# Performance work log

Measured on AMD Instinct MI355X. Metric: run time of the kernel, lower is better.

## Reference

```python
import jax, jax.numpy as jnp
import numpy as np

NUM_NODES = 100000
NUM_EDGES = 1600000
NUM_GRAPHS = 512
IN_F = 128
BN_EPS = 1e-5


def setup_inputs() -> dict:
    key = jax.random.key(0)
    ks = jax.random.split(key, 8)
    x = jax.random.normal(ks[0], (NUM_NODES, IN_F), dtype=jnp.float32)
    edge_index = jax.random.randint(ks[1], (2, NUM_EDGES), 0, NUM_NODES, dtype=jnp.int64)
    batch = jnp.sort(jax.random.randint(ks[2], (NUM_NODES,), 0, NUM_GRAPHS, dtype=jnp.int64))

    def glorot(k, shape):
        lim = np.sqrt(6.0 / (shape[0] + shape[1]))
        return jax.random.uniform(k, shape, jnp.float32, -lim, lim)

    return {
        "x": x,
        "edge_index": edge_index,
        "batch": batch,
        "W1": glorot(ks[3], (IN_F, 128)),
        "b1": jnp.zeros((128,), jnp.float32),
        "W2": glorot(ks[4], (128, 64)),
        "b2": jnp.zeros((64,), jnp.float32),
        "gamma": jnp.ones((64,), jnp.float32),
        "beta": jnp.zeros((64,), jnp.float32),
        "Wo1": glorot(ks[5], (64, 24)),
        "bo1": jnp.zeros((24,), jnp.float32),
        "Wo2": glorot(ks[6], (24, 1)),
        "bo2": jnp.zeros((1,), jnp.float32),
    }


def gcn_conv(x, src, dst, W, b, n):
    # PyG GCNConv: add self-loops, symmetric D^{-1/2} A D^{-1/2} normalization,
    # linear transform, scatter-add aggregation at destination, then bias.
    deg = jax.ops.segment_sum(jnp.ones_like(dst, jnp.float32), dst, num_segments=n)
    dis = jnp.where(deg > 0, jax.lax.rsqrt(deg), 0.0)
    norm = dis[src] * dis[dst]  # [E+N]
    xw = x @ W                  # [N, out]
    msg = xw[src] * norm[:, None]
    return jax.ops.segment_sum(msg, dst, num_segments=n) + b


def reference(x, edge_index, batch, W1, b1, W2, b2, gamma, beta, Wo1, bo1, Wo2, bo2):
    n = NUM_NODES
    loop = jnp.arange(n, dtype=edge_index.dtype)
    src = jnp.concatenate([edge_index[0], loop])  # self-loops appended
    dst = jnp.concatenate([edge_index[1], loop])

    h1 = jax.nn.relu(gcn_conv(x, src, dst, W1, b1, n))
    h2 = jax.nn.relu(gcn_conv(h1, src, dst, W2, b2, n))

    pooled = jax.ops.segment_sum(h2, batch, num_segments=NUM_GRAPHS)  # [G, 64]
    h = jax.lax.stop_gradient(pooled)

    # BatchNorm1d in training mode: batch statistics over the graph dim.
    mean = jnp.mean(pooled, axis=0)
    var = jnp.var(pooled, axis=0)
    xn = (pooled - mean) * jax.lax.rsqrt(var + BN_EPS) * gamma + beta

    out = jax.nn.relu(xn @ Wo1 + bo1) @ Wo2 + bo2  # [G, 1]
    return out, h
```

## Files before the change

### kernel.cpp

```cpp
#include <hip/hip_runtime.h>
#include <math.h>

#define N_NODES 100000
#define N_EDGES 1600000
#define N_GRAPHS 512
#define BN_EPS 1e-5f

#define NBUCKET 1024
#define NBUCKET_USED ((N_NODES + 127) / 128)
#define BCHUNK 8192
#define NCHUNKS ((N_EDGES + BCHUNK - 1) / BCHUNK)

typedef unsigned int uint;
typedef unsigned short ushort;
typedef _Float16 f16;
typedef _Float16 f16x8 __attribute__((ext_vector_type(8)));
typedef float f32x4 __attribute__((ext_vector_type(4)));

constexpr size_t OFF_BCNT  = 0;
constexpr size_t OFF_BCUR  = 4096;
constexpr size_t OFF_BBASE = 8192;
constexpr size_t OFF_DIS   = 12288;
constexpr size_t OFF_ROW   = 412288;
constexpr size_t OFF_SC    = 812416;
constexpr size_t OFF_SH    = 812672;
constexpr size_t OFF_WT    = 812928;
constexpr size_t OFF_CSR   = 862080;
constexpr size_t OFF_P     = 7262080;
constexpr size_t OFF_Q     = 32862080;

__device__ __forceinline__ uint packf16(float a, float b) {
    union { f16 h[2]; uint u; } z;
    z.h[0] = (f16)a; z.h[1] = (f16)b;
    return z.u;
}
__device__ __forceinline__ float2 unpackf16(uint u) {
    union { uint u; f16 h[2]; } z;
    z.u = u;
    return make_float2((float)z.h[0], (float)z.h[1]);
}

__global__ __launch_bounds__(256) void bucket_hist(const int* __restrict__ dst,
                                                   int* __restrict__ bcnt) {
    __shared__ int h[NBUCKET];
    for (int i = threadIdx.x; i < NBUCKET; i += 256) h[i] = 0;
    __syncthreads();
    int stride = gridDim.x * 256;
    for (int e = blockIdx.x * 256 + threadIdx.x; e < N_EDGES; e += stride)
        atomicAdd(&h[dst[e] >> 7], 1);
    __syncthreads();
    for (int i = threadIdx.x; i < NBUCKET; i += 256) {
        int v = h[i];
        if (v) atomicAdd(&bcnt[i], v);
    }
}

__global__ __launch_bounds__(1024) void scan_buckets(const int* __restrict__ bcnt,
                                                     int* __restrict__ bcur,
                                                     int* __restrict__ bbase) {
    __shared__ int tmp[NBUCKET];
    int t = threadIdx.x;
    int c = bcnt[t];
    tmp[t] = c;
    __syncthreads();
    for (int off = 1; off < NBUCKET; off <<= 1) {
        int add = (t >= off) ? tmp[t - off] : 0;
        __syncthreads();
        tmp[t] += add;
        __syncthreads();
    }
    bcur[t] = tmp[t] - c;
    bbase[t] = tmp[t] - c;
}

__global__ __launch_bounds__(1024) void bin_scatter(const int* __restrict__ src,
                                                    const int* __restrict__ dst,
                                                    int* __restrict__ bcur,
                                                    uint* __restrict__ binned) {
    constexpr int REG = BCHUNK / 1024;
    __shared__ int hist[NBUCKET];
    __shared__ int base[NBUCKET];
    int t = threadIdx.x;
    int e0 = blockIdx.x * BCHUNK;
    int lim = N_EDGES - e0;

    hist[t] = 0;
    __syncthreads();

    int ds[REG], ss[REG];
#pragma unroll
    for (int i = 0; i < REG; ++i) {
        int idx = t + i * 1024;
        if (idx < lim) {
            ds[i] = dst[e0 + idx];
            ss[i] = src[e0 + idx];
            atomicAdd(&hist[ds[i] >> 7], 1);
        }
    }
    __syncthreads();

    int h = hist[t];
    base[t] = h ? atomicAdd(&bcur[t], h) : 0;
    hist[t] = 0;
    __syncthreads();

#pragma unroll
    for (int i = 0; i < REG; ++i) {
        int idx = t + i * 1024;
        if (idx < lim) {
            int b = ds[i] >> 7;
            int pos = base[b] + atomicAdd(&hist[b], 1);
            binned[pos] = ((uint)ss[i] << 7) | (uint)(ds[i] & 127);
        }
    }
}

__global__ __launch_bounds__(256) void csr_from_bins(const uint* __restrict__ binned,
                                                     const int* __restrict__ bbase,
                                                     const int* __restrict__ bcnt,
                                                     int* __restrict__ row_start,
                                                     float* __restrict__ dis,
                                                     int* __restrict__ csr_src) {
    __shared__ int cnt[128];
    __shared__ int ex[128];
    int t = threadIdx.x;
    int b = blockIdx.x;
    if (t < 128) cnt[t] = 0;
    __syncthreads();
    int start = bbase[b];
    int end = start + bcnt[b];
    for (int i = start + t; i < end; i += 256)
        atomicAdd(&cnt[binned[i] & 127u], 1);
    __syncthreads();
    if (t < 128) ex[t] = cnt[t];
    __syncthreads();
    for (int off = 1; off < 128; off <<= 1) {
        int v = (t < 128 && t >= off) ? ex[t - off] : 0;
        __syncthreads();
        if (t < 128) ex[t] += v;
        __syncthreads();
    }
    if (t < 128) {
        int c = cnt[t];
        ex[t] -= c;
        int node = b * 128 + t;
        if (node < N_NODES) {
            row_start[node] = start + ex[t];
            dis[node] = rsqrtf((float)(c + 1));
        }
        cnt[t] = 0;
    }
    if (b == 0 && t == 0) row_start[N_NODES] = N_EDGES;
    __syncthreads();
    for (int i = start + t; i < end; i += 256) {
        uint p = binned[i];
        int s = (int)(p >> 7);
        int d = (int)(p & 127u);
        int pos = start + ex[d] + atomicAdd(&cnt[d], 1);
        csr_src[pos] = s;
    }
}

__global__ __launch_bounds__(256) void prep_w(const float* __restrict__ W1,
                                              const float* __restrict__ W2,
                                              f16* __restrict__ wT) {
    int tid = blockIdx.x * 256 + threadIdx.x;
    if (tid < 16384) {
        int n = tid >> 7, k = tid & 127;
        wT[tid] = (f16)W1[k * 128 + n];
    } else if (tid < 24576) {
        int t = tid - 16384;
        int n = t >> 7, k = t & 127;
        wT[tid] = (f16)W2[k * 64 + n];
    }
}

__global__ __launch_bounds__(256) void gemm_mfma1(const float* __restrict__ X,
                                                  const float* __restrict__ dis,
                                                  const f16* __restrict__ Bt,
                                                  ushort* __restrict__ Y) {
    constexpr int NT = 8;
    constexpr int PITCH = 136;
    __shared__ f16 sA[64 * PITCH];
    __shared__ f16 sB[128 * PITCH];
    int tid = threadIdx.x;
    int n0 = blockIdx.x * 64;

    for (int i = tid; i < 64 * 16; i += 256) {
        int r = i >> 4, c = i & 15;
        int n = n0 + r;
        uint4 pk = make_uint4(0, 0, 0, 0);
        if (n < N_NODES) {
            const float4* px = (const float4*)(X + (size_t)n * 128);
            float4 u = px[c * 2], v = px[c * 2 + 1];
            float d = dis[n];
            pk.x = packf16(u.x * d, u.y * d);
            pk.y = packf16(u.z * d, u.w * d);
            pk.z = packf16(v.x * d, v.y * d);
            pk.w = packf16(v.z * d, v.w * d);
        }
        *(uint4*)&sA[r * PITCH + c * 8] = pk;
    }
    for (int i = tid; i < 128 * 16; i += 256) {
        int r = i >> 4, c = i & 15;
        *(uint4*)&sB[r * PITCH + c * 8] = ((const uint4*)(Bt + r * 128))[c];
    }
    __syncthreads();

    int lane = tid & 63, wave = tid >> 6;
    int l15 = lane & 15, q = lane >> 4;
    int m0 = wave * 16;
    f32x4 acc[NT];
#pragma unroll
    for (int nt = 0; nt < NT; ++nt) acc[nt] = (f32x4){0.f, 0.f, 0.f, 0.f};

    const f16* pa = &sA[(m0 + l15) * PITCH + q * 8];
    const f16* pb = &sB[l15 * PITCH + q * 8];
#pragma unroll
    for (int kk = 0; kk < 4; ++kk) {
        f16x8 a = *(const f16x8*)(pa + kk * 32);
#pragma unroll
        for (int nt = 0; nt < NT; ++nt) {
            f16x8 b = *(const f16x8*)(pb + nt * 16 * PITCH + kk * 32);
            acc[nt] = __builtin_amdgcn_mfma_f32_16x16x32_f16(a, b, acc[nt], 0, 0, 0);
        }
    }

    int row_base = n0 + m0 + q * 4;
#pragma unroll
    for (int nt = 0; nt < NT; ++nt) {
#pragma unroll
        for (int r = 0; r < 4; ++r) {
            int row = row_base + r;
            if (row < N_NODES) {
                union { f16 h; ushort u; } z;
                z.h = (f16)acc[nt][r];
                Y[(size_t)row * 128 + nt * 16 + l15] = z.u;
            }
        }
    }
}

template <int OUTF>
__global__ __launch_bounds__(256) void gemm_mfma(const f16* __restrict__ A,
                                                 const f16* __restrict__ Bt,
                                                 ushort* __restrict__ Y) {
    constexpr int NT = OUTF / 16;
    constexpr int PITCH = 136;
    __shared__ f16 sA[64 * PITCH];
    __shared__ f16 sB[OUTF * PITCH];
    int tid = threadIdx.x;
    int n0 = blockIdx.x * 64;

    for (int i = tid; i < 64 * 16; i += 256) {
        int r = i >> 4, c = i & 15;
        int n = n0 + r;
        uint4 v = make_uint4(0, 0, 0, 0);
        if (n < N_NODES) v = ((const uint4*)(A + (size_t)n * 128))[c];
        *(uint4*)&sA[r * PITCH + c * 8] = v;
    }
    for (int i = tid; i < OUTF * 16; i += 256) {
        int r = i >> 4, c = i & 15;
        *(uint4*)&sB[r * PITCH + c * 8] = ((const uint4*)(Bt + r * 128))[c];
    }
    __syncthreads();

    int lane = tid & 63, wave = tid >> 6;
    int l15 = lane & 15, q = lane >> 4;
    int m0 = wave * 16;
    f32x4 acc[NT];
#pragma unroll
    for (int nt = 0; nt < NT; ++nt) acc[nt] = (f32x4){0.f, 0.f, 0.f, 0.f};

    const f16* pa = &sA[(m0 + l15) * PITCH + q * 8];
    const f16* pb = &sB[l15 * PITCH + q * 8];
#pragma unroll
    for (int kk = 0; kk < 4; ++kk) {
        f16x8 a = *(const f16x8*)(pa + kk * 32);
#pragma unroll
        for (int nt = 0; nt < NT; ++nt) {
            f16x8 b = *(const f16x8*)(pb + nt * 16 * PITCH + kk * 32);
            acc[nt] = __builtin_amdgcn_mfma_f32_16x16x32_f16(a, b, acc[nt], 0, 0, 0);
        }
    }

    int row_base = n0 + m0 + q * 4;
#pragma unroll
    for (int nt = 0; nt < NT; ++nt) {
#pragma unroll
        for (int r = 0; r < 4; ++r) {
            int row = row_base + r;
            if (row < N_NODES) {
                union { f16 h; ushort u; } z;
                z.h = (f16)acc[nt][r];
                Y[(size_t)row * OUTF + nt * 16 + l15] = z.u;
            }
        }
    }
}

__global__ __launch_bounds__(256) void aggregate1(const ushort* __restrict__ M,
                                                  const int* __restrict__ row_start,
                                                  const int* __restrict__ csr_src,
                                                  const float* __restrict__ dis,
                                                  const float* __restrict__ bias,
                                                  ushort* __restrict__ H1s) {
    int wv = __builtin_amdgcn_readfirstlane((int)(threadIdx.x >> 6));
    int n = blockIdx.x * 4 + wv;
    if (n >= N_NODES) return;
    int lane = threadIdx.x & 63;
    float dn = dis[n];
    int e0 = row_start[n], e1 = row_start[n + 1];
    const uint* rows = (const uint*)M;
    float2 t0 = unpackf16(rows[(size_t)n * 64 + lane]);
    float a0 = t0.x, a1 = t0.y, b0 = 0.f, b1v = 0.f;
    int e = e0;
    for (; e + 16 <= e1; e += 16) {
        int s[16];
#pragma unroll
        for (int j = 0; j < 16; ++j) s[j] = csr_src[e + j];
        uint v[16];
#pragma unroll
        for (int j = 0; j < 16; ++j) v[j] = rows[(size_t)s[j] * 64 + lane];
#pragma unroll
        for (int j = 0; j < 16; ++j) {
            float2 f = unpackf16(v[j]);
            if (j & 1) { b0 += f.x; b1v += f.y; } else { a0 += f.x; a1 += f.y; }
        }
    }
    for (; e + 8 <= e1; e += 8) {
        int s[8];
#pragma unroll
        for (int j = 0; j < 8; ++j) s[j] = csr_src[e + j];
        uint v[8];
#pragma unroll
        for (int j = 0; j < 8; ++j) v[j] = rows[(size_t)s[j] * 64 + lane];
#pragma unroll
        for (int j = 0; j < 8; ++j) {
            float2 f = unpackf16(v[j]);
            if (j & 1) { b0 += f.x; b1v += f.y; } else { a0 += f.x; a1 += f.y; }
        }
    }
    for (; e + 4 <= e1; e += 4) {
        int s0 = csr_src[e], s1 = csr_src[e + 1], s2 = csr_src[e + 2], s3 = csr_src[e + 3];
        uint v0 = rows[(size_t)s0 * 64 + lane];
        uint v1 = rows[(size_t)s1 * 64 + lane];
        uint v2 = rows[(size_t)s2 * 64 + lane];
        uint v3 = rows[(size_t)s3 * 64 + lane];
        float2 f0 = unpackf16(v0), f1 = unpackf16(v1), f2 = unpackf16(v2), f3 = unpackf16(v3);
        a0 += f0.x + f1.x; a1 += f0.y + f1.y;
        b0 += f2.x + f3.x; b1v += f2.y + f3.y;
    }
    for (; e < e1; ++e) {
        float2 f = unpackf16(rows[(size_t)csr_src[e] * 64 + lane]);
        a0 += f.x; a1 += f.y;
    }
    a0 += b0; a1 += b1v;
    a0 = fmaxf(fmaf(a0, dn, bias[2 * lane]), 0.f) * dn;
    a1 = fmaxf(fmaf(a1, dn, bias[2 * lane + 1]), 0.f) * dn;
    ((uint*)H1s)[(size_t)n * 64 + lane] = packf16(a0, a1);
}

__global__ __launch_bounds__(256) void aggregate2(const ushort* __restrict__ M,
                                                  const int* __restrict__ row_start,
                                                  const int* __restrict__ csr_src,
                                                  const float* __restrict__ dis,
                                                  const float* __restrict__ bias,
                                                  float* __restrict__ out) {
    int wv = __builtin_amdgcn_readfirstlane((int)(threadIdx.x >> 6));
    int n = blockIdx.x * 4 + wv;
    if (n >= N_NODES) return;
    int lane = threadIdx.x & 63;
    float dn = dis[n];
    int e0 = row_start[n], e1 = row_start[n + 1];
    const f16* rows = (const f16*)M;
    float a0 = (float)rows[(size_t)n * 64 + lane];
    float a1 = 0.f;
    int e = e0;
    for (; e + 16 <= e1; e += 16) {
        int s[16];
#pragma unroll
        for (int j = 0; j < 16; ++j) s[j] = csr_src[e + j];
        f16 v[16];
#pragma unroll
        for (int j = 0; j < 16; ++j) v[j] = rows[(size_t)s[j] * 64 + lane];
#pragma unroll
        for (int j = 0; j < 16; ++j) {
            if (j & 1) a1 += (float)v[j]; else a0 += (float)v[j];
        }
    }
    for (; e + 8 <= e1; e += 8) {
        int s[8];
#pragma unroll
        for (int j = 0; j < 8; ++j) s[j] = csr_src[e + j];
        f16 v[8];
#pragma unroll
        for (int j = 0; j < 8; ++j) v[j] = rows[(size_t)s[j] * 64 + lane];
#pragma unroll
        for (int j = 0; j < 8; ++j) {
            if (j & 1) a1 += (float)v[j]; else a0 += (float)v[j];
        }
    }
    for (; e + 4 <= e1; e += 4) {
        int s0 = csr_src[e], s1 = csr_src[e + 1], s2 = csr_src[e + 2], s3 = csr_src[e + 3];
        float v0 = (float)rows[(size_t)s0 * 64 + lane];
        float v1 = (float)rows[(size_t)s1 * 64 + lane];
        float v2 = (float)rows[(size_t)s2 * 64 + lane];
        float v3 = (float)rows[(size_t)s3 * 64 + lane];
        a0 += v0 + v1; a1 += v2 + v3;
    }
    for (; e < e1; ++e) a0 += (float)rows[(size_t)csr_src[e] * 64 + lane];
    a0 += a1;
    a0 = fmaf(a0, dn, bias[lane]);
    out[(size_t)n * 64 + lane] = fmaxf(a0, 0.f);
}

__global__ __launch_bounds__(64) void pool_graphs(const float* __restrict__ H,
                                                  const int* __restrict__ batch,
                                                  float* __restrict__ pooled) {
    int g = blockIdx.x;
    int lane = threadIdx.x;
    int lo = 0, hi = N_NODES;
    while (lo < hi) { int mid = (lo + hi) >> 1; if (batch[mid] < g) lo = mid + 1; else hi = mid; }
    int start = lo;
    hi = N_NODES;
    while (lo < hi) { int mid = (lo + hi) >> 1; if (batch[mid] < g + 1) lo = mid + 1; else hi = mid; }
    int end = lo;
    float a0 = 0.f, a1 = 0.f;
    int i = start;
    for (; i + 4 <= end; i += 4) {
        a0 += H[(size_t)i * 64 + lane] + H[(size_t)(i + 1) * 64 + lane];
        a1 += H[(size_t)(i + 2) * 64 + lane] + H[(size_t)(i + 3) * 64 + lane];
    }
    for (; i < end; ++i) a0 += H[(size_t)i * 64 + lane];
    pooled[g * 64 + lane] = a0 + a1;
}

__global__ __launch_bounds__(64) void bn_stats(const float* __restrict__ pooled,
                                               const float* __restrict__ gamma,
                                               const float* __restrict__ beta,
                                               float* __restrict__ scale,
                                               float* __restrict__ shift) {
    int f = threadIdx.x;
    float s = 0.f, s2 = 0.f;
    for (int g = 0; g < N_GRAPHS; ++g) {
        float v = pooled[g * 64 + f];
        s += v;
        s2 = fmaf(v, v, s2);
    }
    float mean = s * (1.0f / N_GRAPHS);
    float var = s2 * (1.0f / N_GRAPHS) - mean * mean;
    float istd = rsqrtf(var + BN_EPS);
    float sc = gamma[f] * istd;
    scale[f] = sc;
    shift[f] = beta[f] - mean * sc;
}

__global__ __launch_bounds__(256) void head(const float* __restrict__ pooled,
                                            const float* __restrict__ scale,
                                            const float* __restrict__ shift,
                                            const float* __restrict__ Wo1,
                                            const float* __restrict__ bo1,
                                            const float* __restrict__ Wo2,
                                            const float* __restrict__ bo2,
                                            float* __restrict__ out) {
    __shared__ float sW1[64 * 24];
    __shared__ float sW2[24];
    __shared__ float sb1[24];
    __shared__ float ssc[64];
    __shared__ float ssh[64];
    int tid = threadIdx.x;
    for (int i = tid; i < 64 * 24; i += 256) sW1[i] = Wo1[i];
    if (tid < 24) { sW2[tid] = Wo2[tid]; sb1[tid] = bo1[tid]; }
    if (tid < 64) { ssc[tid] = scale[tid]; ssh[tid] = shift[tid]; }
    __syncthreads();
    int g = blockIdx.x * 256 + tid;
    if (g >= N_GRAPHS) return;
    float xn[64];
    const float* pr = pooled + g * 64;
#pragma unroll
    for (int j = 0; j < 64; ++j) xn[j] = fmaf(pr[j], ssc[j], ssh[j]);
    float o = bo2[0];
#pragma unroll 4
    for (int k = 0; k < 24; ++k) {
        float h = sb1[k];
#pragma unroll
        for (int j = 0; j < 64; ++j) h = fmaf(xn[j], sW1[j * 24 + k], h);
        o = fmaf(fmaxf(h, 0.f), sW2[k], o);
    }
    out[g] = o;
}

extern "C" void kernel_launch(void* const* d_in, const int* in_sizes, int n_in,
                              void* d_out, int out_size, void* d_ws, size_t ws_size,
                              hipStream_t stream) {
    const float* x     = (const float*)d_in[0];
    const int*   ei    = (const int*)d_in[1];
    const int*   batch = (const int*)d_in[2];
    const float* W1    = (const float*)d_in[3];
    const float* b1    = (const float*)d_in[4];
    const float* W2    = (const float*)d_in[5];
    const float* b2    = (const float*)d_in[6];
    const float* gamma = (const float*)d_in[7];
    const float* beta  = (const float*)d_in[8];
    const float* Wo1   = (const float*)d_in[9];
    const float* bo1   = (const float*)d_in[10];
    const float* Wo2   = (const float*)d_in[11];
    const float* bo2   = (const float*)d_in[12];
    float* out = (float*)d_out;
    char* ws = (char*)d_ws;

    const int* srcv = ei;
    const int* dstv = ei + N_EDGES;
    int*    bcnt     = (int*)(ws + OFF_BCNT);
    int*    bcur     = (int*)(ws + OFF_BCUR);
    int*    bbase    = (int*)(ws + OFF_BBASE);
    float*  dis      = (float*)(ws + OFF_DIS);
    int*    row_start= (int*)(ws + OFF_ROW);
    float*  scale    = (float*)(ws + OFF_SC);
    float*  shift    = (float*)(ws + OFF_SH);
    f16*    wT       = (f16*)(ws + OFF_WT);
    int*    csr_src  = (int*)(ws + OFF_CSR);
    f16*    bufP     = (f16*)(ws + OFF_P);
    ushort* bufQ     = (ushort*)(ws + OFF_Q);
    uint*   binned   = (uint*)(ws + OFF_Q);
    float*  pooled   = out + N_GRAPHS;

    hipMemsetAsync(ws + OFF_BCNT, 0, 4096, stream);

    bucket_hist<<<256, 256, 0, stream>>>(dstv, bcnt);
    scan_buckets<<<1, NBUCKET, 0, stream>>>(bcnt, bcur, bbase);
    bin_scatter<<<NCHUNKS, 1024, 0, stream>>>(srcv, dstv, bcur, binned);
    csr_from_bins<<<NBUCKET_USED, 256, 0, stream>>>(binned, bbase, bcnt, row_start, dis, csr_src);

    prep_w<<<96, 256, 0, stream>>>(W1, W2, wT);

    int gblocks = (N_NODES + 63) / 64;
    int ablocks = (N_NODES + 3) / 4;
    gemm_mfma1<<<gblocks, 256, 0, stream>>>(x, dis, wT, bufQ);
    aggregate1<<<ablocks, 256, 0, stream>>>(bufQ, row_start, csr_src, dis, b1, (ushort*)bufP);
    gemm_mfma<64><<<gblocks, 256, 0, stream>>>(bufP, wT + 16384, bufQ);
    aggregate2<<<ablocks, 256, 0, stream>>>(bufQ, row_start, csr_src, dis, b2, (float*)bufP);

    pool_graphs<<<N_GRAPHS, 64, 0, stream>>>((float*)bufP, batch, pooled);
    bn_stats<<<1, 64, 0, stream>>>(pooled, gamma, beta, scale, shift);
    head<<<2, 256, 0, stream>>>(pooled, scale, shift, Wo1, bo1, Wo2, bo2, out);
}
```

Baseline: 336.0 us.

## Fuse layer-1 aggregation with layer-2 GEMM and merge BN stats into head

```diff
diff --git a/kernel.cpp b/kernel.cpp
--- a/kernel.cpp
+++ b/kernel.cpp
@@ -22,8 +22,6 @@
 constexpr size_t OFF_BBASE = 8192;
 constexpr size_t OFF_DIS   = 12288;
 constexpr size_t OFF_ROW   = 412288;
-constexpr size_t OFF_SC    = 812416;
-constexpr size_t OFF_SH    = 812672;
 constexpr size_t OFF_WT    = 812928;
 constexpr size_t OFF_CSR   = 862080;
 constexpr size_t OFF_P     = 7262080;
@@ -241,124 +239,99 @@
     }
 }
 
-template <int OUTF>
-__global__ __launch_bounds__(256) void gemm_mfma(const f16* __restrict__ A,
-                                                 const f16* __restrict__ Bt,
-                                                 ushort* __restrict__ Y) {
-    constexpr int NT = OUTF / 16;
+__global__ __launch_bounds__(256) void aggregate1_fused(const ushort* __restrict__ M,
+                                                        const int* __restrict__ row_start,
+                                                        const int* __restrict__ csr_src,
+                                                        const float* __restrict__ dis,
+                                                        const float* __restrict__ bias,
+                                                        const f16* __restrict__ W2t,
+                                                        ushort* __restrict__ M2) {
     constexpr int PITCH = 136;
-    __shared__ f16 sA[64 * PITCH];
-    __shared__ f16 sB[OUTF * PITCH];
+    constexpr int HP = 130;
+    __shared__ f16 sB[64 * PITCH];
+    __shared__ f16 sH[16 * HP];
     int tid = threadIdx.x;
-    int n0 = blockIdx.x * 64;
-
     for (int i = tid; i < 64 * 16; i += 256) {
         int r = i >> 4, c = i & 15;
+        *(uint4*)&sB[r * PITCH + c * 8] = ((const uint4*)(W2t + r * 128))[c];
+    }
+    int wv = __builtin_amdgcn_readfirstlane((int)(tid >> 6));
+    int lane = tid & 63;
+    int n0 = blockIdx.x * 16;
+    const uint* rows = (const uint*)M;
+
+    for (int i = 0; i < 4; ++i) {
+        int r = wv * 4 + i;
         int n = n0 + r;
-        uint4 v = make_uint4(0, 0, 0, 0);
-        if (n < N_NODES) v = ((const uint4*)(A + (size_t)n * 128))[c];
-        *(uint4*)&sA[r * PITCH + c * 8] = v;
-    }
-    for (int i = tid; i < OUTF * 16; i += 256) {
-        int r = i >> 4, c = i & 15;
-        *(uint4*)&sB[r * PITCH + c * 8] = ((const uint4*)(Bt + r * 128))[c];
-    }
-    __syncthreads();
-
-    int lane = tid & 63, wave = tid >> 6;
+        float dn = dis[n];
+        int e0 = row_start[n], e1 = row_start[n + 1];
+        float2 t0 = unpackf16(rows[(size_t)n * 64 + lane]);
+        float a0 = t0.x, a1 = t0.y, b0 = 0.f, b1v = 0.f;
+        int e = e0;
+        for (; e + 16 <= e1; e += 16) {
+            int s[16];
+#pragma unroll
+            for (int j = 0; j < 16; ++j) s[j] = csr_src[e + j];
+            uint v[16];
+#pragma unroll
+            for (int j = 0; j < 16; ++j) v[j] = rows[(size_t)s[j] * 64 + lane];
+#pragma unroll
+            for (int j = 0; j < 16; ++j) {
+                float2 f = unpackf16(v[j]);
+                if (j & 1) { b0 += f.x; b1v += f.y; } else { a0 += f.x; a1 += f.y; }
+            }
+        }
+        for (; e + 8 <= e1; e += 8) {
+            int s[8];
+#pragma unroll
+            for (int j = 0; j < 8; ++j) s[j] = csr_src[e + j];
+            uint v[8];
+#pragma unroll
+            for (int j = 0; j < 8; ++j) v[j] = rows[(size_t)s[j] * 64 + lane];
+#pragma unroll
+            for (int j = 0; j < 8; ++j) {
+                float2 f = unpackf16(v[j]);
+                if (j & 1) { b0 += f.x; b1v += f.y; } else { a0 += f.x; a1 += f.y; }
+            }
+        }
+        for (; e + 4 <= e1; e += 4) {
+            int s0 = csr_src[e], s1 = csr_src[e + 1], s2 = csr_src[e + 2], s3 = csr_src[e + 3];
+            uint v0 = rows[(size_t)s0 * 64 + lane];
+            uint v1 = rows[(size_t)s1 * 64 + lane];
+            uint v2 = rows[(size_t)s2 * 64 + lane];
+            uint v3 = rows[(size_t)s3 * 64 + lane];
+            float2 f0 = unpackf16(v0), f1 = unpackf16(v1), f2 = unpackf16(v2), f3 = unpackf16(v3);
+            a0 += f0.x + f1.x; a1 += f0.y + f1.y;
+            b0 += f2.x + f3.x; b1v += f2.y + f3.y;
+        }
+        for (; e < e1; ++e) {
+            float2 f = unpackf16(rows[(size_t)csr_src[e] * 64 + lane]);
+            a0 += f.x; a1 += f.y;
+        }
+        a0 += b0; a1 += b1v;
+        a0 = fmaxf(fmaf(a0, dn, bias[2 * lane]), 0.f) * dn;
+        a1 = fmaxf(fmaf(a1, dn, bias[2 * lane + 1]), 0.f) * dn;
+        *(uint*)&sH[r * HP + 2 * lane] = packf16(a0, a1);
+    }
+    __syncthreads();
+
     int l15 = lane & 15, q = lane >> 4;
-    int m0 = wave * 16;
-    f32x4 acc[NT];
-#pragma unroll
-    for (int nt = 0; nt < NT; ++nt) acc[nt] = (f32x4){0.f, 0.f, 0.f, 0.f};
-
-    const f16* pa = &sA[(m0 + l15) * PITCH + q * 8];
-    const f16* pb = &sB[l15 * PITCH + q * 8];
+    f32x4 acc = (f32x4){0.f, 0.f, 0.f, 0.f};
+    const f16* pa = &sH[l15 * HP + q * 8];
+    const f16* pb = &sB[(wv * 16 + l15) * PITCH + q * 8];
 #pragma unroll
     for (int kk = 0; kk < 4; ++kk) {
         f16x8 a = *(const f16x8*)(pa + kk * 32);
-#pragma unroll
-        for (int nt = 0; nt < NT; ++nt) {
-            f16x8 b = *(const f16x8*)(pb + nt * 16 * PITCH + kk * 32);
-            acc[nt] = __builtin_amdgcn_mfma_f32_16x16x32_f16(a, b, acc[nt], 0, 0, 0);
-        }
-    }
-
-    int row_base = n0 + m0 + q * 4;
-#pragma unroll
-    for (int nt = 0; nt < NT; ++nt) {
-#pragma unroll
-        for (int r = 0; r < 4; ++r) {
-            int row = row_base + r;
-            if (row < N_NODES) {
-                union { f16 h; ushort u; } z;
-                z.h = (f16)acc[nt][r];
-                Y[(size_t)row * OUTF + nt * 16 + l15] = z.u;
-            }
-        }
-    }
-}
-
-__global__ __launch_bounds__(256) void aggregate1(const ushort* __restrict__ M,
-                                                  const int* __restrict__ row_start,
-                                                  const int* __restrict__ csr_src,
-                                                  const float* __restrict__ dis,
-                                                  const float* __restrict__ bias,
-                                                  ushort* __restrict__ H1s) {
-    int wv = __builtin_amdgcn_readfirstlane((int)(threadIdx.x >> 6));
-    int n = blockIdx.x * 4 + wv;
-    if (n >= N_NODES) return;
-    int lane = threadIdx.x & 63;
-    float dn = dis[n];
-    int e0 = row_start[n], e1 = row_start[n + 1];
-    const uint* rows = (const uint*)M;
-    float2 t0 = unpackf16(rows[(size_t)n * 64 + lane]);
-    float a0 = t0.x, a1 = t0.y, b0 = 0.f, b1v = 0.f;
-    int e = e0;
-    for (; e + 16 <= e1; e += 16) {
-        int s[16];
-#pragma unroll
-        for (int j = 0; j < 16; ++j) s[j] = csr_src[e + j];
-        uint v[16];
-#pragma unroll
-        for (int j = 0; j < 16; ++j) v[j] = rows[(size_t)s[j] * 64 + lane];
-#pragma unroll
-        for (int j = 0; j < 16; ++j) {
-            float2 f = unpackf16(v[j]);
-            if (j & 1) { b0 += f.x; b1v += f.y; } else { a0 += f.x; a1 += f.y; }
-        }
-    }
-    for (; e + 8 <= e1; e += 8) {
-        int s[8];
-#pragma unroll
-        for (int j = 0; j < 8; ++j) s[j] = csr_src[e + j];
-        uint v[8];
-#pragma unroll
-        for (int j = 0; j < 8; ++j) v[j] = rows[(size_t)s[j] * 64 + lane];
-#pragma unroll
-        for (int j = 0; j < 8; ++j) {
-            float2 f = unpackf16(v[j]);
-            if (j & 1) { b0 += f.x; b1v += f.y; } else { a0 += f.x; a1 += f.y; }
-        }
-    }
-    for (; e + 4 <= e1; e += 4) {
-        int s0 = csr_src[e], s1 = csr_src[e + 1], s2 = csr_src[e + 2], s3 = csr_src[e + 3];
-        uint v0 = rows[(size_t)s0 * 64 + lane];
-        uint v1 = rows[(size_t)s1 * 64 + lane];
-        uint v2 = rows[(size_t)s2 * 64 + lane];
-        uint v3 = rows[(size_t)s3 * 64 + lane];
-        float2 f0 = unpackf16(v0), f1 = unpackf16(v1), f2 = unpackf16(v2), f3 = unpackf16(v3);
-        a0 += f0.x + f1.x; a1 += f0.y + f1.y;
-        b0 += f2.x + f3.x; b1v += f2.y + f3.y;
-    }
-    for (; e < e1; ++e) {
-        float2 f = unpackf16(rows[(size_t)csr_src[e] * 64 + lane]);
-        a0 += f.x; a1 += f.y;
-    }
-    a0 += b0; a1 += b1v;
-    a0 = fmaxf(fmaf(a0, dn, bias[2 * lane]), 0.f) * dn;
-    a1 = fmaxf(fmaf(a1, dn, bias[2 * lane + 1]), 0.f) * dn;
-    ((uint*)H1s)[(size_t)n * 64 + lane] = packf16(a0, a1);
+        f16x8 b = *(const f16x8*)(pb + kk * 32);
+        acc = __builtin_amdgcn_mfma_f32_16x16x32_f16(a, b, acc, 0, 0, 0);
+    }
+    int row_base = n0 + q * 4;
+#pragma unroll
+    for (int rr = 0; rr < 4; ++rr) {
+        union { f16 h; ushort u; } z;
+        z.h = (f16)acc[rr];
+        M2[(size_t)(row_base + rr) * 64 + wv * 16 + l15] = z.u;
+    }
 }
 
 __global__ __launch_bounds__(256) void aggregate2(const ushort* __restrict__ M,
@@ -436,46 +409,38 @@
     pooled[g * 64 + lane] = a0 + a1;
 }
 
-__global__ __launch_bounds__(64) void bn_stats(const float* __restrict__ pooled,
+__global__ __launch_bounds__(512) void bn_head(const float* __restrict__ pooled,
                                                const float* __restrict__ gamma,
                                                const float* __restrict__ beta,
-                                               float* __restrict__ scale,
-                                               float* __restrict__ shift) {
-    int f = threadIdx.x;
-    float s = 0.f, s2 = 0.f;
-    for (int g = 0; g < N_GRAPHS; ++g) {
-        float v = pooled[g * 64 + f];
-        s += v;
-        s2 = fmaf(v, v, s2);
-    }
-    float mean = s * (1.0f / N_GRAPHS);
-    float var = s2 * (1.0f / N_GRAPHS) - mean * mean;
-    float istd = rsqrtf(var + BN_EPS);
-    float sc = gamma[f] * istd;
-    scale[f] = sc;
-    shift[f] = beta[f] - mean * sc;
-}
-
-__global__ __launch_bounds__(256) void head(const float* __restrict__ pooled,
-                                            const float* __restrict__ scale,
-                                            const float* __restrict__ shift,
-                                            const float* __restrict__ Wo1,
-                                            const float* __restrict__ bo1,
-                                            const float* __restrict__ Wo2,
-                                            const float* __restrict__ bo2,
-                                            float* __restrict__ out) {
+                                               const float* __restrict__ Wo1,
+                                               const float* __restrict__ bo1,
+                                               const float* __restrict__ Wo2,
+                                               const float* __restrict__ bo2,
+                                               float* __restrict__ out) {
     __shared__ float sW1[64 * 24];
     __shared__ float sW2[24];
     __shared__ float sb1[24];
     __shared__ float ssc[64];
     __shared__ float ssh[64];
     int tid = threadIdx.x;
-    for (int i = tid; i < 64 * 24; i += 256) sW1[i] = Wo1[i];
-    if (tid < 24) { sW2[tid] = Wo2[tid]; sb1[tid] = bo1[tid]; }
-    if (tid < 64) { ssc[tid] = scale[tid]; ssh[tid] = shift[tid]; }
-    __syncthreads();
-    int g = blockIdx.x * 256 + tid;
-    if (g >= N_GRAPHS) return;
+    for (int i = tid; i < 64 * 24; i += 512) sW1[i] = Wo1[i];
+    if (tid >= 64 && tid < 88) { int k = tid - 64; sW2[k] = Wo2[k]; sb1[k] = bo1[k]; }
+    if (tid < 64) {
+        float s = 0.f, s2 = 0.f;
+        for (int g = 0; g < N_GRAPHS; ++g) {
+            float v = pooled[g * 64 + tid];
+            s += v;
+            s2 = fmaf(v, v, s2);
+        }
+        float mean = s * (1.0f / N_GRAPHS);
+        float var = s2 * (1.0f / N_GRAPHS) - mean * mean;
+        float istd = rsqrtf(var + BN_EPS);
+        float sc = gamma[tid] * istd;
+        ssc[tid] = sc;
+        ssh[tid] = beta[tid] - mean * sc;
+    }
+    __syncthreads();
+    int g = tid;
     float xn[64];
     const float* pr = pooled + g * 64;
 #pragma unroll
@@ -517,11 +482,9 @@
     int*    bbase    = (int*)(ws + OFF_BBASE);
     float*  dis      = (float*)(ws + OFF_DIS);
     int*    row_start= (int*)(ws + OFF_ROW);
-    float*  scale    = (float*)(ws + OFF_SC);
-    float*  shift    = (float*)(ws + OFF_SH);
     f16*    wT       = (f16*)(ws + OFF_WT);
     int*    csr_src  = (int*)(ws + OFF_CSR);
-    f16*    bufP     = (f16*)(ws + OFF_P);
+    ushort* bufP     = (ushort*)(ws + OFF_P);
     ushort* bufQ     = (ushort*)(ws + OFF_Q);
     uint*   binned   = (uint*)(ws + OFF_Q);
     float*  pooled   = out + N_GRAPHS;
@@ -536,13 +499,12 @@
     prep_w<<<96, 256, 0, stream>>>(W1, W2, wT);
 
     int gblocks = (N_NODES + 63) / 64;
-    int ablocks = (N_NODES + 3) / 4;
     gemm_mfma1<<<gblocks, 256, 0, stream>>>(x, dis, wT, bufQ);
-    aggregate1<<<ablocks, 256, 0, stream>>>(bufQ, row_start, csr_src, dis, b1, (ushort*)bufP);
-    gemm_mfma<64><<<gblocks, 256, 0, stream>>>(bufP, wT + 16384, bufQ);
-    aggregate2<<<ablocks, 256, 0, stream>>>(bufQ, row_start, csr_src, dis, b2, (float*)bufP);
-
-    pool_graphs<<<N_GRAPHS, 64, 0, stream>>>((float*)bufP, batch, pooled);
-    bn_stats<<<1, 64, 0, stream>>>(pooled, gamma, beta, scale, shift);
-    head<<<2, 256, 0, stream>>>(pooled, scale, shift, Wo1, bo1, Wo2, bo2, out);
-}
+    aggregate1_fused<<<N_NODES / 16, 256, 0, stream>>>(bufQ, row_start, csr_src, dis, b1,
+                                                       wT + 16384, bufP);
+    aggregate2<<<(N_NODES + 3) / 4, 256, 0, stream>>>(bufP, row_start, csr_src, dis, b2,
+                                                      (float*)bufQ);
+
+    pool_graphs<<<N_GRAPHS, 64, 0, stream>>>((float*)bufQ, batch, pooled);
+    bn_head<<<1, 512, 0, stream>>>(pooled, gamma, beta, Wo1, bo1, Wo2, bo2, out);
+}
```

New measurement: 329.8 us. No clear change (-1.8%).
